# Kernel optimization log

Measured on AMD Instinct MI355X. Metric: run time of the kernel, lower is better.

Reference implementation:

```python
import jax, jax.numpy as jnp
import numpy as np

D = 256
H = 4
L = 6
N = 32768
NH = N // H  # 8192 per-head width
VOCAB = 256
B, T = 1, 1024
ROPE_BASE = 10000.0


def ln(x):
    # LayerNorm over last dim, no affine (elementwise_affine=False)
    m = jnp.mean(x, axis=-1, keepdims=True)
    v = jnp.var(x, axis=-1, keepdims=True)
    return (x - m) * jax.lax.rsqrt(v + 1e-5)


def rope(x):
    # standard rotary position embedding over the last dim (split-half convention)
    Dh = x.shape[-1]
    t = x.shape[-2]
    half = Dh // 2
    inv_freq = 1.0 / (ROPE_BASE ** (jnp.arange(half, dtype=jnp.float32) / half))
    ang = jnp.arange(t, dtype=jnp.float32)[:, None] * inv_freq[None, :]  # [T, half]
    cos, sin = jnp.cos(ang), jnp.sin(ang)
    x1, x2 = x[..., :half], x[..., half:]
    return jnp.concatenate([x1 * cos - x2 * sin, x2 * cos + x1 * sin], axis=-1)


def setup_inputs() -> dict:
    key = jax.random.key(0)
    ks = jax.random.split(key, 6)
    std = 0.02
    return {
        "idx": jax.random.randint(ks[0], (B, T), 0, VOCAB, dtype=jnp.int32),
        "wte": std * jax.random.normal(ks[1], (VOCAB, D), dtype=jnp.float32),
        "encoder": std * jax.random.normal(ks[2], (N, D), dtype=jnp.float32),
        "decoder_x": std * jax.random.normal(ks[3], (H, D, NH), dtype=jnp.float32),
        "decoder_y": std * jax.random.normal(ks[4], (H, D, NH), dtype=jnp.float32),
        "readout": std * jax.random.normal(ks[5], (D, VOCAB), dtype=jnp.float32),
    }


def reference(idx, wte, encoder, decoder_x, decoder_y, readout):
    b, t = idx.shape
    v = ln(wte[idx])  # [B, T, D]
    # strict causal mask (tril with diagonal=-1): position i attends to j < i
    mask = jnp.tril(jnp.ones((t, t), dtype=bool), k=-1)
    for _ in range(L):
        # x: relu(v @ decoder_x) -> [B, H, T, NH]
        x = jax.nn.relu(jnp.einsum('btd,hdn->bhtn', v, decoder_x))
        xr = rope(x)  # Q = K = x
        # unnormalized causal linear attention, strict lower triangular
        scores = jnp.einsum('bhtn,bhsn->bhts', xr, xr)
        scores = jnp.where(mask, scores, 0.0)
        a = jnp.einsum('bhts,bsd->bhtd', scores, v)  # V = v (broadcast over heads)
        # gated wide projection
        y = jax.nn.relu(jnp.einsum('bhtd,hdn->bhtn', ln(a), decoder_y)) * x
        # [B,H,T,NH] -> [B,T,H*NH] = [B,T,N]  (matches transpose(1,2).reshape)
        y = jnp.transpose(y, (0, 2, 1, 3)).reshape(b, t, N)
        v = ln(v + ln(y @ encoder))  # dropout is identity in eval
    return v @ readout  # [B, T, VOCAB]
```

## Files before the change

### kernel.cpp

```cpp
#include <hip/hip_runtime.h>
#include <hip/hip_bf16.h>
#include <stdint.h>

typedef unsigned short u16;
typedef unsigned int u32;
typedef __attribute__((ext_vector_type(8))) short i16x8;
typedef __attribute__((ext_vector_type(4))) float f32x4;

#define DEV __device__ __forceinline__

constexpr int T = 1024, D = 256, H = 4, NH = 8192, NF = 32768, HALF = 4096;

constexpr size_t OFF_DXT  = 0;
constexpr size_t OFF_DYT  = OFF_DXT  + (size_t)H*NH*D*2;
constexpr size_t OFF_ENCT = OFF_DYT  + (size_t)H*NH*D*2;
constexpr size_t OFF_ROT  = OFF_ENCT + (size_t)D*NF*2;
constexpr size_t OFF_COS  = OFF_ROT  + (size_t)D*D*2;
constexpr size_t OFF_SIN  = OFF_COS  + (size_t)T*HALF*4;
constexpr size_t OFF_V    = OFF_SIN  + (size_t)T*HALF*4;
constexpr size_t OFF_VBF  = OFF_V    + (size_t)T*D*4;
constexpr size_t OFF_VT   = OFF_VBF  + (size_t)T*D*2;
constexpr size_t OFF_X    = OFF_VT   + (size_t)T*D*2;
constexpr size_t OFF_XR   = OFF_X    + (size_t)T*NF*2;
constexpr size_t OFF_SC   = OFF_XR   + (size_t)T*NF*2;
constexpr size_t OFF_LA   = OFF_SC   + (size_t)H*T*T*2;
constexpr size_t OFF_PART = OFF_LA   + (size_t)H*T*D*2;
constexpr size_t WS_NEED  = OFF_PART + (size_t)8*T*T*4;


DEV u16 f2bf(float f) {
  u32 u = __float_as_uint(f);
  u += 0x7FFFu + ((u >> 16) & 1u);
  return (u16)(u >> 16);
}
DEV float bf2f(u16 u) { return __uint_as_float(((u32)u) << 16); }

DEV float2 block_sum2(float a, float b, float* sb) {
  #pragma unroll
  for (int o = 32; o > 0; o >>= 1) {
    a += __shfl_down(a, o, 64);
    b += __shfl_down(b, o, 64);
  }
  const int w = threadIdx.x >> 6;
  __syncthreads();
  if ((threadIdx.x & 63) == 0) { sb[w*2] = a; sb[w*2+1] = b; }
  __syncthreads();
  return make_float2(sb[0]+sb[2]+sb[4]+sb[6], sb[1]+sb[3]+sb[5]+sb[7]);
}

DEV void stage128(const u16* __restrict__ g, int ld, char* lds, int wave, int lane) {
  #pragma unroll
  for (int i = 0; i < 4; ++i) {
    const int f = (wave*4 + i)*64 + lane;
    const int row = f >> 3, seg = f & 7;
    const int segl = seg ^ (row & 7);
    const u16* src = g + (size_t)row*ld + segl*8;
    __builtin_amdgcn_global_load_lds(
        (const __attribute__((address_space(1))) void*)src,
        (__attribute__((address_space(3))) void*)(lds + ((wave*4 + i) << 10)),
        16, 0, 0);
  }
}

DEV void mfma_tile(const char* Ac, const char* Bc, int wm, int wn, int lr, int lk,
                   f32x4 acc[4][4]) {
  #pragma unroll
  for (int kk = 0; kk < 2; ++kk) {
    const int lcol = kk*64 + lk*16;
    i16x8 af[4], bfv[4];
    #pragma unroll
    for (int m = 0; m < 4; ++m) {
      const int row = wm*64 + m*16 + lr;
      af[m] = *(const i16x8*)(Ac + row*128 + (lcol ^ ((row & 7) << 4)));
    }
    #pragma unroll
    for (int n = 0; n < 4; ++n) {
      const int row = wn*64 + n*16 + lr;
      bfv[n] = *(const i16x8*)(Bc + row*128 + (lcol ^ ((row & 7) << 4)));
    }
    #pragma unroll
    for (int m = 0; m < 4; ++m)
      #pragma unroll
      for (int n = 0; n < 4; ++n)
        acc[m][n] = __builtin_amdgcn_mfma_f32_16x16x32_bf16(af[m], bfv[n], acc[m][n], 0, 0, 0);
  }
}

DEV void gemm_bt_core(const u16* __restrict__ Ab, int lda,
                      const u16* __restrict__ Bb, int ldb,
                      int nkt, char* smem, f32x4 acc[4][4]) {
  const int tid = threadIdx.x, lane = tid & 63, wave = tid >> 6;
  const int wm = wave >> 1, wn = wave & 1;
  const int lr = lane & 15, lk = lane >> 4;
  char* As = smem;
  char* Bs = smem + 32768;
  #pragma unroll
  for (int m = 0; m < 4; ++m)
    #pragma unroll
    for (int n = 0; n < 4; ++n) acc[m][n] = f32x4{0.f, 0.f, 0.f, 0.f};
  stage128(Ab, lda, As, wave, lane);
  stage128(Bb, ldb, Bs, wave, lane);
  __syncthreads();
  for (int kt = 0; kt < nkt; ++kt) {
    const int cur = kt & 1;
    if (kt + 1 < nkt) {
      stage128(Ab + (size_t)(kt+1)*64, lda, As + ((cur^1) << 14), wave, lane);
      stage128(Bb + (size_t)(kt+1)*64, ldb, Bs + ((cur^1) << 14), wave, lane);
    }
    mfma_tile(As + (cur << 14), Bs + (cur << 14), wm, wn, lr, lk, acc);
    __syncthreads();
  }
}

DEV void gemm_bt_core_sb(const u16* __restrict__ Ab, int lda,
                         const u16* __restrict__ Bb, int ldb,
                         int nkt, char* smem, f32x4 acc[4][4]) {
  const int tid = threadIdx.x, lane = tid & 63, wave = tid >> 6;
  const int wm = wave >> 1, wn = wave & 1;
  const int lr = lane & 15, lk = lane >> 4;
  char* As = smem;
  char* Bs = smem + 16384;
  #pragma unroll
  for (int m = 0; m < 4; ++m)
    #pragma unroll
    for (int n = 0; n < 4; ++n) acc[m][n] = f32x4{0.f, 0.f, 0.f, 0.f};
  for (int kt = 0; kt < nkt; ++kt) {
    stage128(Ab + (size_t)kt*64, lda, As, wave, lane);
    stage128(Bb + (size_t)kt*64, ldb, Bs, wave, lane);
    __syncthreads();
    mfma_tile(As, Bs, wm, wn, lr, lk, acc);
    __syncthreads();
  }
}

#define EPILOG_IDX() \
  const int lane = threadIdx.x & 63, wave = threadIdx.x >> 6; \
  const int wm = wave >> 1, wn = wave & 1, lr = lane & 15, lk = lane >> 4; \
  const int r0 = wm*64 + lk*4; \
  const int c0 = wn*64 + lr;

constexpr int TS = 136;

template<int MODE>
DEV void store_tile_sb(const f32x4 acc[4][4], u16* __restrict__ dst, int ld,
                       const u16* __restrict__ xg, char* smem) {
  u16* tb = (u16*)smem;
  const int lane = threadIdx.x & 63, wave = threadIdx.x >> 6;
  const int wm = wave >> 1, wn = wave & 1, lr = lane & 15, lk = lane >> 4;
  const int c0 = wn*64 + lr, rb = lk*4;
  const int rr = threadIdx.x >> 4, cc = (threadIdx.x & 15)*8;
  #pragma unroll
  for (int half = 0; half < 2; ++half) {
    if (wm == half) {
      #pragma unroll
      for (int m = 0; m < 4; ++m)
        #pragma unroll
        for (int n = 0; n < 4; ++n)
          #pragma unroll
          for (int r = 0; r < 4; ++r) {
            float v = acc[m][n][r];
            if (MODE >= 1) v = fmaxf(v, 0.f);
            tb[(size_t)(rb + m*16 + r)*TS + c0 + n*16] = f2bf(v);
          }
    }
    __syncthreads();
    #pragma unroll
    for (int it = 0; it < 4; ++it) {
      const int row = it*16 + rr;
      const int grow = half*64 + row;
      i16x8 w = *(const i16x8*)(tb + (size_t)row*TS + cc);
      if (MODE == 2) {
        const i16x8 xv = *(const i16x8*)(xg + (size_t)grow*ld + cc);
        #pragma unroll
        for (int j = 0; j < 8; ++j)
          w[j] = (short)f2bf(bf2f((u16)w[j]) * bf2f((u16)xv[j]));
      }
      *(i16x8*)(dst + (size_t)grow*ld + cc) = w;
    }
    __syncthreads();
  }
}

template<int PERM>
__global__ __launch_bounds__(256) void k_transpose_cvt(const float* __restrict__ in,
                                                       u16* __restrict__ out, int R, int C) {
  __shared__ float tile[32][33];
  const size_t zoff = (size_t)blockIdx.z * R * C;
  const float* inz = in + zoff;
  u16* outz = out + zoff;
  const int c0 = blockIdx.x << 5, rr0 = blockIdx.y << 5;
  const int tx = threadIdx.x & 31, ty = threadIdx.x >> 5;
  #pragma unroll
  for (int i = 0; i < 4; ++i) {
    int irow = rr0 + ty + i*8;
    if (PERM == 2) {
      const int hh = irow >> 13, j = irow & 8191;
      irow = hh*8192 + ((j & 1) ? (j >> 1) + 4096 : (j >> 1));
    }
    tile[ty + i*8][tx] = inz[(size_t)irow*C + c0 + tx];
  }
  __syncthreads();
  #pragma unroll
  for (int i = 0; i < 4; ++i) {
    const int rr = ty + i*8;
    int orow = c0 + rr;
    if (PERM == 1) {
      const int j = orow & 8191;
      orow = (orow & ~8191) | ((j < 4096) ? 2*j : 2*(j - 4096) + 1);
    }
    outz[(size_t)orow*R + rr0 + tx] = f2bf(tile[tx][rr]);
  }
}

__global__ __launch_bounds__(256) void k_rope_table(float* __restrict__ cosT,
                                                    float* __restrict__ sinT) {
  const int i = blockIdx.x*256 + threadIdx.x;
  const int t = blockIdx.y;
  const float p = (float)i * (1.f/4096.f);
  const float ang = (float)t * expf(-9.210340371976184f * p);
  cosT[(size_t)t*HALF + i] = cosf(ang);
  sinT[(size_t)t*HALF + i] = sinf(ang);
}

__global__ __launch_bounds__(256) void k_embed(const int* __restrict__ idx,
                                               const float* __restrict__ wte,
                                               float* __restrict__ v,
                                               u16* __restrict__ vbf, u16* __restrict__ vT) {
  __shared__ float sb[8];
  const int t = blockIdx.x, d = threadIdx.x;
  const float val = wte[(size_t)idx[t]*D + d];
  float2 ss = block_sum2(val, val*val, sb);
  const float m = ss.x*(1.f/256.f), var = ss.y*(1.f/256.f) - m*m;
  const float vn = (val - m) * rsqrtf(var + 1e-5f);
  v[(size_t)t*D + d] = vn;
  const u16 b = f2bf(vn);
  vbf[(size_t)t*D + d] = b;
  vT[(size_t)d*T + t] = b;
}

__global__ __launch_bounds__(256) void k_gemm_x_rope(const u16* __restrict__ vbf,
                                                     const u16* __restrict__ dxT,
                                                     u16* __restrict__ x,
                                                     u16* __restrict__ xr,
                                                     const float* __restrict__ cosT,
                                                     const float* __restrict__ sinT) {
  __shared__ char smem[32768];
  const int p = blockIdx.x;
  const int slot = p & 7;
  const int h = (p >> 3) & 3;
  const int seq = p >> 5;
  const int nt = slot*8 + (seq & 7);
  const int mt = seq >> 3;
  f32x4 acc[4][4];
  gemm_bt_core_sb(vbf + (size_t)mt*128*D, D,
                  dxT + ((size_t)h*NH + (size_t)nt*128)*D, D, 4, smem, acc);
  u16* tb = (u16*)smem;
  const int lane = threadIdx.x & 63, wave = threadIdx.x >> 6;
  const int wm = wave >> 1, wn = wave & 1, lr = lane & 15, lk = lane >> 4;
  const int c0 = wn*64 + lr, rb = lk*4;
  const int rr = threadIdx.x >> 4, cc = (threadIdx.x & 15)*8;
  const size_t obase = (size_t)mt*128*NF + (size_t)h*NH + (size_t)nt*128;
  const int pbase = (nt*128 + cc) >> 1;
  #pragma unroll
  for (int half = 0; half < 2; ++half) {
    if (wm == half) {
      #pragma unroll
      for (int m = 0; m < 4; ++m)
        #pragma unroll
        for (int n = 0; n < 4; ++n)
          #pragma unroll
          for (int r = 0; r < 4; ++r)
            tb[(size_t)(rb + m*16 + r)*TS + c0 + n*16] = f2bf(fmaxf(acc[m][n][r], 0.f));
    }
    __syncthreads();
    #pragma unroll
    for (int it = 0; it < 4; ++it) {
      const int row = it*16 + rr;
      const int grow = half*64 + row;
      const i16x8 w = *(const i16x8*)(tb + (size_t)row*TS + cc);
      *(i16x8*)(x + obase + (size_t)grow*NF + cc) = w;
      const int t = mt*128 + grow;
      const float4 cv = *(const float4*)(cosT + (size_t)t*HALF + pbase);
      const float4 sv = *(const float4*)(sinT + (size_t)t*HALF + pbase);
      i16x8 rg;
      float x1, x2;
      x1 = bf2f((u16)w[0]); x2 = bf2f((u16)w[1]);
      rg[0] = (short)f2bf(x1*cv.x - x2*sv.x); rg[1] = (short)f2bf(x2*cv.x + x1*sv.x);
      x1 = bf2f((u16)w[2]); x2 = bf2f((u16)w[3]);
      rg[2] = (short)f2bf(x1*cv.y - x2*sv.y); rg[3] = (short)f2bf(x2*cv.y + x1*sv.y);
      x1 = bf2f((u16)w[4]); x2 = bf2f((u16)w[5]);
      rg[4] = (short)f2bf(x1*cv.z - x2*sv.z); rg[5] = (short)f2bf(x2*cv.z + x1*sv.z);
      x1 = bf2f((u16)w[6]); x2 = bf2f((u16)w[7]);
      rg[6] = (short)f2bf(x1*cv.w - x2*sv.w); rg[7] = (short)f2bf(x2*cv.w + x1*sv.w);
      *(i16x8*)(xr + obase + (size_t)grow*NF + cc) = rg;
    }
    __syncthreads();
  }
}

__global__ __launch_bounds__(256) void k_gemm_sc(const u16* __restrict__ xr,
                                                 u16* __restrict__ scb) {
  __shared__ char smem[32768];
  const int z = blockIdx.x & 15;
  const int i = blockIdx.x >> 4;
  int tt = 0;
  while ((tt + 1)*(tt + 2)/2 <= i) ++tt;
  const int st = i - tt*(tt + 1)/2;
  const int h = z >> 2, kc = z & 3;
  const u16* base = xr + (size_t)h*NH + (size_t)kc*2048;
  f32x4 acc[4][4];
  gemm_bt_core_sb(base + (size_t)tt*128*NF, NF, base + (size_t)st*128*NF, NF, 32, smem, acc);
  store_tile_sb<0>(acc, scb + (size_t)z*T*T + (size_t)tt*128*T + (size_t)st*128, T,
                   nullptr, smem);
}

__global__ __launch_bounds__(256) void k_sc_combine(const u16* __restrict__ scb,
                                                    u16* __restrict__ sc) {
  const int row = blockIdx.x;
  const int h = row >> 10, t = row & 1023;
  const u16* p0 = scb + ((size_t)(h*4 + 0)*T + t)*T;
  u16* o = sc + (size_t)row*T;
  const int s0 = threadIdx.x*4;
  ushort4 r;
  if (s0 >= t) {
    r.x = 0; r.y = 0; r.z = 0; r.w = 0;
  } else {
    const ushort4 a0 = *(const ushort4*)(p0 + s0);
    const ushort4 a1 = *(const ushort4*)(p0 + T*T + s0);
    const ushort4 a2 = *(const ushort4*)(p0 + 2*(size_t)T*T + s0);
    const ushort4 a3 = *(const ushort4*)(p0 + 3*(size_t)T*T + s0);
    const float vx = bf2f(a0.x) + bf2f(a1.x) + bf2f(a2.x) + bf2f(a3.x);
    const float vy = bf2f(a0.y) + bf2f(a1.y) + bf2f(a2.y) + bf2f(a3.y);
    const float vz = bf2f(a0.z) + bf2f(a1.z) + bf2f(a2.z) + bf2f(a3.z);
    const float vw = bf2f(a0.w) + bf2f(a1.w) + bf2f(a2.w) + bf2f(a3.w);
    r.x = f2bf((s0 + 0 < t) ? vx : 0.f);
    r.y = f2bf((s0 + 1 < t) ? vy : 0.f);
    r.z = f2bf((s0 + 2 < t) ? vz : 0.f);
    r.w = f2bf((s0 + 3 < t) ? vw : 0.f);
  }
  *(ushort4*)(o + s0) = r;
}

__global__ __launch_bounds__(256) void k_gemm_av(const u16* __restrict__ sc,
                                                 const u16* __restrict__ vT,
                                                 float* __restrict__ part) {
  __shared__ char smem[65536];
  const int slot = blockIdx.x & 7;
  const int h = slot >> 1, nt = slot & 1;
  int mt = 0, kc = 0, rem = blockIdx.x >> 3;
  #pragma unroll
  for (int m = 0; m < 8; ++m) {
    const int c = (m >> 1) + 1;
    if (rem < c) { mt = m; kc = rem; break; }
    rem -= c;
  }
  f32x4 acc[4][4];
  gemm_bt_core(sc + ((size_t)h*T + (size_t)mt*128)*T + (size_t)kc*256, T,
               vT + (size_t)nt*128*T + (size_t)kc*256, T, 4, smem, acc);
  EPILOG_IDX();
  float* Cp = part + (size_t)(h*4 + kc) * T * D;
  const int tb = mt*128 + r0, cb = nt*128 + c0;
  #pragma unroll
  for (int m = 0; m < 4; ++m)
    #pragma unroll
    for (int n = 0; n < 4; ++n)
      #pragma unroll
      for (int r = 0; r < 4; ++r)
        Cp[(size_t)(tb + m*16 + r)*D + cb + n*16] = acc[m][n][r];
}

__global__ __launch_bounds__(256) void k_ln_a(const float* __restrict__ part,
                                              u16* __restrict__ la) {
  __shared__ float sb[8];
  const int row = blockIdx.x;
  const int h = row >> 10, t = row & 1023;
  const int d = threadIdx.x;
  const int nkc = ((t >> 7) >> 1) + 1;
  float s = 0.f;
  for (int kc = 0; kc < nkc; ++kc)
    s += part[((size_t)(h*4 + kc)*T + t)*D + d];
  float2 ss = block_sum2(s, s*s, sb);
  const float m = ss.x*(1.f/256.f), var = ss.y*(1.f/256.f) - m*m;
  la[(size_t)row*D + d] = f2bf((s - m) * rsqrtf(var + 1e-5f));
}

__global__ __launch_bounds__(256) void k_gemm_y(const u16* __restrict__ la,
                                                const u16* __restrict__ dyT,
                                                const u16* __restrict__ x,
                                                u16* __restrict__ y) {
  __shared__ char smem[32768];
  const int nt = blockIdx.x, mt = blockIdx.y, h = blockIdx.z;
  f32x4 acc[4][4];
  gemm_bt_core_sb(la + ((size_t)h*T + (size_t)mt*128)*D, D,
                  dyT + ((size_t)h*NH + (size_t)nt*128)*D, D, 4, smem, acc);
  const size_t off = (size_t)mt*128*NF + (size_t)h*NH + (size_t)nt*128;
  store_tile_sb<2>(acc, y + off, NF, x + off, smem);
}

__global__ __launch_bounds__(256) void k_gemm_enc(const u16* __restrict__ y,
                                                  const u16* __restrict__ encT,
                                                  float* __restrict__ part) {
  __shared__ char smem[65536];
  const int slot = blockIdx.x & 7;
  const int seq  = blockIdx.x >> 3;
  const int kcc = slot*4 + (seq >> 4);
  const int nt = seq & 1;
  const int mt = (seq >> 1) & 7;
  f32x4 acc[4][4];
  gemm_bt_core(y + (size_t)mt*128*NF + (size_t)kcc*1024, NF,
               encT + (size_t)nt*128*NF + (size_t)kcc*1024, NF, 16, smem, acc);
  EPILOG_IDX();
  float* Cp = part + (size_t)kcc * T * D;
  const int tb = mt*128 + r0, cb = nt*128 + c0;
  #pragma unroll
  for (int m = 0; m < 4; ++m)
    #pragma unroll
    for (int n = 0; n < 4; ++n)
      #pragma unroll
      for (int r = 0; r < 4; ++r)
        Cp[(size_t)(tb + m*16 + r)*D + cb + n*16] = acc[m][n][r];
}

__global__ __launch_bounds__(256) void k_newv(const float* __restrict__ part,
                                              float* __restrict__ v,
                                              u16* __restrict__ vbf, u16* __restrict__ vT) {
  __shared__ float sb[8];
  const int t = blockIdx.x, d = threadIdx.x;
  float s = 0.f;
  #pragma unroll
  for (int kc = 0; kc < 32; ++kc)
    s += part[((size_t)kc*T + t)*D + d];
  float2 ss = block_sum2(s, s*s, sb);
  float m = ss.x*(1.f/256.f), var = ss.y*(1.f/256.f) - m*m;
  const float l1 = (s - m) * rsqrtf(var + 1e-5f);
  const float u = v[(size_t)t*D + d] + l1;
  float2 s2 = block_sum2(u, u*u, sb);
  m = s2.x*(1.f/256.f); var = s2.y*(1.f/256.f) - m*m;
  const float vn = (u - m) * rsqrtf(var + 1e-5f);
  v[(size_t)t*D + d] = vn;
  const u16 bb = f2bf(vn);
  vbf[(size_t)t*D + d] = bb;
  vT[(size_t)d*T + t] = bb;
}

__global__ __launch_bounds__(256) void k_gemm_out(const u16* __restrict__ vbf,
                                                  const u16* __restrict__ roT,
                                                  float* __restrict__ out) {
  __shared__ char smem[65536];
  const int nt = blockIdx.x, mt = blockIdx.y;
  f32x4 acc[4][4];
  gemm_bt_core(vbf + (size_t)mt*128*D, D, roT + (size_t)nt*128*D, D, 4, smem, acc);
  EPILOG_IDX();
  const int tb = mt*128 + r0, cb = nt*128 + c0;
  #pragma unroll
  for (int m = 0; m < 4; ++m)
    #pragma unroll
    for (int n = 0; n < 4; ++n)
      #pragma unroll
      for (int r = 0; r < 4; ++r)
        out[(size_t)(tb + m*16 + r)*D + cb + n*16] = acc[m][n][r];
}

extern "C" void kernel_launch(void* const* d_in, const int* in_sizes, int n_in,
                              void* d_out, int out_size, void* d_ws, size_t ws_size,
                              hipStream_t stream) {
  (void)in_sizes; (void)n_in; (void)out_size; (void)ws_size;
  const int*   idx = (const int*)d_in[0];
  const float* wte = (const float*)d_in[1];
  const float* enc = (const float*)d_in[2];
  const float* dx  = (const float*)d_in[3];
  const float* dy  = (const float*)d_in[4];
  const float* ro  = (const float*)d_in[5];
  float* out = (float*)d_out;
  char* ws = (char*)d_ws;

  u16* dxT  = (u16*)(ws + OFF_DXT);
  u16* dyT  = (u16*)(ws + OFF_DYT);
  u16* encT = (u16*)(ws + OFF_ENCT);
  u16* roT  = (u16*)(ws + OFF_ROT);
  float* cosT = (float*)(ws + OFF_COS);
  float* sinT = (float*)(ws + OFF_SIN);
  float* v    = (float*)(ws + OFF_V);
  u16* vbf  = (u16*)(ws + OFF_VBF);
  u16* vT   = (u16*)(ws + OFF_VT);
  u16* x    = (u16*)(ws + OFF_X);
  u16* xr   = (u16*)(ws + OFF_XR);
  u16* sc   = (u16*)(ws + OFF_SC);
  u16* la   = (u16*)(ws + OFF_LA);
  u16* scb  = (u16*)(ws + OFF_PART);
  float* part = (float*)(ws + OFF_PART);

  k_transpose_cvt<1><<<dim3(NH/32, D/32, H), 256, 0, stream>>>(dx, dxT, D, NH);
  k_transpose_cvt<1><<<dim3(NH/32, D/32, H), 256, 0, stream>>>(dy, dyT, D, NH);
  k_transpose_cvt<2><<<dim3(D/32, NF/32, 1), 256, 0, stream>>>(enc, encT, NF, D);
  k_transpose_cvt<0><<<dim3(D/32, D/32, 1), 256, 0, stream>>>(ro, roT, D, D);
  k_rope_table<<<dim3(HALF/256, T), 256, 0, stream>>>(cosT, sinT);
  k_embed<<<T, 256, 0, stream>>>(idx, wte, v, vbf, vT);

  for (int l = 0; l < 6; ++l) {
    k_gemm_x_rope<<<2048,          256, 0, stream>>>(vbf, dxT, x, xr, cosT, sinT);
    k_gemm_sc <<<576,              256, 0, stream>>>(xr, scb);
    k_sc_combine<<<H*T,            256, 0, stream>>>(scb, sc);
    k_gemm_av <<<160,              256, 0, stream>>>(sc, vT, part);
    k_ln_a    <<<H*T,              256, 0, stream>>>(part, la);
    k_gemm_y  <<<dim3(64, 8, H),   256, 0, stream>>>(la, dyT, x, xr );
    k_gemm_enc<<<512,              256, 0, stream>>>(xr , encT, part);
    k_newv    <<<T,                256, 0, stream>>>(part, v, vbf, vT);
  }
  k_gemm_out<<<dim3(2, 8), 256, 0, stream>>>(vbf, roT, out);
}
```

Baseline: 1.320 ms.

## Split score GEMM tiles to 128x64 with double-buffered direct-to-LDS K=32 staging

The causal score GEMM now uses 128x64 output tiles instead of 128x128, doubling the grid to 1152 blocks. A new core loads K-slices of 32 straight into LDS with a swizzled layout and double-buffers them, so the next slice's loads overlap the current MFMA work and only one barrier is needed per step. This targets latency and occupancy in the score kernel. In exchange, A tiles are reloaded twice as often and each block does more, smaller iterations.

```diff
diff --git a/kernel.cpp b/kernel.cpp
--- a/kernel.cpp
+++ b/kernel.cpp
@@ -130,6 +130,99 @@
     __syncthreads();
     mfma_tile(As, Bs, wm, wn, lr, lk, acc);
     __syncthreads();
+  }
+}
+
+DEV void stageA32(const u16* __restrict__ g, int ld, char* lds, int tid) {
+  #pragma unroll
+  for (int i = 0; i < 2; ++i) {
+    const int f = i*256 + tid;
+    const int row = f >> 2;
+    const int segl = (f & 3) ^ (row & 3);
+    const u16* src = g + (size_t)row*ld + segl*8;
+    __builtin_amdgcn_global_load_lds(
+        (const __attribute__((address_space(1))) void*)src,
+        (__attribute__((address_space(3))) void*)(lds + ((size_t)f << 4)),
+        16, 0, 0);
+  }
+}
+DEV void stageB32(const u16* __restrict__ g, int ld, char* lds, int tid) {
+  const int f = tid;
+  const int row = f >> 2;
+  const int segl = (f & 3) ^ (row & 3);
+  const u16* src = g + (size_t)row*ld + segl*8;
+  __builtin_amdgcn_global_load_lds(
+      (const __attribute__((address_space(1))) void*)src,
+      (__attribute__((address_space(3))) void*)(lds + ((size_t)f << 4)),
+      16, 0, 0);
+}
+
+DEV void mfma_tile32(const char* Ac, const char* Bc, int wm, int wn, int lr, int lk,
+                     f32x4 acc[4][2]) {
+  const int lcol = lk*16;
+  i16x8 af[4], bfv[2];
+  #pragma unroll
+  for (int m = 0; m < 4; ++m) {
+    const int row = wm*64 + m*16 + lr;
+    af[m] = *(const i16x8*)(Ac + row*64 + (lcol ^ ((row & 3) << 4)));
+  }
+  #pragma unroll
+  for (int n = 0; n < 2; ++n) {
+    const int row = wn*32 + n*16 + lr;
+    bfv[n] = *(const i16x8*)(Bc + row*64 + (lcol ^ ((row & 3) << 4)));
+  }
+  #pragma unroll
+  for (int m = 0; m < 4; ++m)
+    #pragma unroll
+    for (int n = 0; n < 2; ++n)
+      acc[m][n] = __builtin_amdgcn_mfma_f32_16x16x32_bf16(af[m], bfv[n], acc[m][n], 0, 0, 0);
+}
+
+DEV void gemm_bt_core32(const u16* __restrict__ Ab, int lda,
+                        const u16* __restrict__ Bb, int ldb,
+                        int nkt, char* smem, f32x4 acc[4][2]) {
+  const int tid = threadIdx.x, lane = tid & 63, wave = tid >> 6;
+  const int wm = wave >> 1, wn = wave & 1;
+  const int lr = lane & 15, lk = lane >> 4;
+  #pragma unroll
+  for (int m = 0; m < 4; ++m)
+    #pragma unroll
+    for (int n = 0; n < 2; ++n) acc[m][n] = f32x4{0.f, 0.f, 0.f, 0.f};
+  stageA32(Ab, lda, smem, tid);
+  stageB32(Bb, ldb, smem + 8192, tid);
+  __syncthreads();
+  for (int kt = 0; kt < nkt; ++kt) {
+    const int cur = kt & 1;
+    char* bufn = smem + ((cur^1) ? 12288 : 0);
+    if (kt + 1 < nkt) {
+      stageA32(Ab + (size_t)(kt+1)*32, lda, bufn, tid);
+      stageB32(Bb + (size_t)(kt+1)*32, ldb, bufn + 8192, tid);
+    }
+    const char* bufc = smem + (cur ? 12288 : 0);
+    mfma_tile32(bufc, bufc + 8192, wm, wn, lr, lk, acc);
+    __syncthreads();
+  }
+}
+
+DEV void store_tile64(const f32x4 acc[4][2], u16* __restrict__ dst, int ld, char* smem) {
+  u16* tb = (u16*)smem;
+  const int lane = threadIdx.x & 63, wave = threadIdx.x >> 6;
+  const int wm = wave >> 1, wn = wave & 1, lr = lane & 15, lk = lane >> 4;
+  const int r0 = wm*64 + lk*4, c0 = wn*32 + lr;
+  #pragma unroll
+  for (int m = 0; m < 4; ++m)
+    #pragma unroll
+    for (int n = 0; n < 2; ++n)
+      #pragma unroll
+      for (int r = 0; r < 4; ++r)
+        tb[(size_t)(r0 + m*16 + r)*72 + c0 + n*16] = f2bf(acc[m][n][r]);
+  __syncthreads();
+  const int rr = threadIdx.x >> 3;
+  const int cc = (threadIdx.x & 7)*8;
+  #pragma unroll
+  for (int it = 0; it < 4; ++it) {
+    const int row = it*32 + rr;
+    *(i16x8*)(dst + (size_t)row*ld + cc) = *(const i16x8*)(tb + (size_t)row*72 + cc);
   }
 }
 
@@ -300,18 +393,21 @@
 
 __global__ __launch_bounds__(256) void k_gemm_sc(const u16* __restrict__ xr,
                                                  u16* __restrict__ scb) {
-  __shared__ char smem[32768];
+  __shared__ char smem[24576];
   const int z = blockIdx.x & 15;
-  const int i = blockIdx.x >> 4;
+  const int j = blockIdx.x >> 4;
+  const int i = j >> 1;
+  const int nh = j & 1;
   int tt = 0;
   while ((tt + 1)*(tt + 2)/2 <= i) ++tt;
   const int st = i - tt*(tt + 1)/2;
   const int h = z >> 2, kc = z & 3;
   const u16* base = xr + (size_t)h*NH + (size_t)kc*2048;
-  f32x4 acc[4][4];
-  gemm_bt_core_sb(base + (size_t)tt*128*NF, NF, base + (size_t)st*128*NF, NF, 32, smem, acc);
-  store_tile_sb<0>(acc, scb + (size_t)z*T*T + (size_t)tt*128*T + (size_t)st*128, T,
-                   nullptr, smem);
+  f32x4 acc[4][2];
+  gemm_bt_core32(base + (size_t)tt*128*NF, NF,
+                 base + ((size_t)st*128 + (size_t)nh*64)*NF, NF, 64, smem, acc);
+  store_tile64(acc, scb + (size_t)z*T*T + (size_t)tt*128*T + (size_t)st*128 + (size_t)nh*64,
+               T, smem);
 }
 
 __global__ __launch_bounds__(256) void k_sc_combine(const u16* __restrict__ scb,
@@ -499,7 +595,7 @@
 
   for (int l = 0; l < 6; ++l) {
     k_gemm_x_rope<<<2048,          256, 0, stream>>>(vbf, dxT, x, xr, cosT, sinT);
-    k_gemm_sc <<<576,              256, 0, stream>>>(xr, scb);
+    k_gemm_sc <<<1152,             256, 0, stream>>>(xr, scb);
     k_sc_combine<<<H*T,            256, 0, stream>>>(scb, sc);
     k_gemm_av <<<160,              256, 0, stream>>>(sc, vT, part);
     k_ln_a    <<<H*T,              256, 0, stream>>>(part, la);
```

Result: faster. 1.270 ms (-3.8%).
